# Kernel optimization log

Hardware: AMD Instinct MI355X
Metric: run time of the kernel (lower is better)

Reference implementation:

```python
import jax, jax.numpy as jnp
import numpy as np

N_NODES = 100000


def setup_inputs() -> dict:
    key = jax.random.key(0)
    k1, k2, k3, k4, k5 = jax.random.split(key, 5)
    n_edges = 3200000
    in_f, out_f = 256, 256
    X = jax.random.normal(k1, (N_NODES, in_f), dtype=jnp.float32)
    edge_src = jax.random.randint(k2, (n_edges,), 0, N_NODES, dtype=jnp.int32)
    edge_dst = jax.random.randint(k3, (n_edges,), 0, N_NODES, dtype=jnp.int32)
    edge_val = jax.random.uniform(k4, (n_edges,), dtype=jnp.float32)
    # kaiming-uniform-like init for weight (out_f, in_f)
    bound = np.sqrt(6.0 / in_f)
    W = jax.random.uniform(k5, (out_f, in_f), dtype=jnp.float32, minval=-bound, maxval=bound)
    b = jnp.zeros((out_f,), dtype=jnp.float32)
    return {"X": X, "edge_src": edge_src, "edge_dst": edge_dst,
            "edge_val": edge_val, "W": W, "b": b}


def reference(X, edge_src, edge_dst, edge_val, W, b):
    # S = A @ X, where A is COO sparse: A[src, dst] = val
    # gather neighbor features, scale by edge value, scatter-add to src rows
    msgs = edge_val[:, None] * X[edge_dst]              # [E, in_f]
    S = jax.ops.segment_sum(msgs, edge_src, num_segments=N_NODES)  # [N, in_f]
    # dense projection + bias: (A X) W^T + b
    return S @ W.T + b
```

## Files before the change

### kernel.cpp

```cpp
#include <hip/hip_runtime.h>

#define NNODES 100000
#define F 256
#define NBKT ((NNODES + 127) / 128)
#define BKT_CAP 5120
#define CHUNK_A 8192

typedef unsigned short u16;
typedef unsigned int   u32;
typedef __attribute__((ext_vector_type(8))) short short8v;
typedef __attribute__((ext_vector_type(8))) unsigned short ushort8;
typedef __attribute__((ext_vector_type(4))) float f32x4;
typedef __attribute__((ext_vector_type(2))) float f32x2;

__device__ __forceinline__ u16 f2bf(float f) {
    u32 u = __float_as_uint(f);
    u32 r = u + 0x7FFFu + ((u >> 16) & 1u);
    return (u16)(r >> 16);
}

__global__ __launch_bounds__(256) void cast_w_init(const float* __restrict__ W,
                                                   u16* __restrict__ Wb,
                                                   int* __restrict__ cur) {
    int i = blockIdx.x * 256 + threadIdx.x;
    if (i < F * F / 4) {
        float4 w = ((const float4*)W)[i];
        ushort4 o;
        o.x = f2bf(w.x); o.y = f2bf(w.y); o.z = f2bf(w.z); o.w = f2bf(w.w);
        ((ushort4*)Wb)[i] = o;
    }
    if (i < NBKT) cur[i] = i * BKT_CAP;
}

__global__ __launch_bounds__(256) void cast_x(const float* __restrict__ X,
                                              u16* __restrict__ Xb, int total4) {
    int i = blockIdx.x * 256 + threadIdx.x;
    if (i >= total4) return;
    float4 x = ((const float4*)X)[i];
    ushort4 o;
    o.x = f2bf(x.x); o.y = f2bf(x.y); o.z = f2bf(x.z); o.w = f2bf(x.w);
    ((ushort4*)Xb)[i] = o;
}

__global__ __launch_bounds__(256) void gemm_mfma(const u16* __restrict__ Xb,
                                                 const u16* __restrict__ Wb,
                                                 u16* __restrict__ Yb) {
    __shared__ u16 As[128 * 128];
    __shared__ u16 Bs[128 * 128];
    const int wv   = threadIdx.x >> 6;
    const int lane = threadIdx.x & 63;
    const int lm   = lane & 15;
    const int kg   = lane >> 4;
    const int m0   = blockIdx.x * 128;
    const int n0   = blockIdx.y * 128;

    f32x4 acc[2][8];
#pragma unroll
    for (int t = 0; t < 2; ++t)
#pragma unroll
        for (int u = 0; u < 8; ++u) acc[t][u] = (f32x4){0.f, 0.f, 0.f, 0.f};

#pragma unroll
    for (int kt = 0; kt < 2; ++kt) {
        if (kt) __syncthreads();
#pragma unroll
        for (int i = 0; i < 8; ++i) {
            int q   = i * 256 + threadIdx.x;
            int row = q >> 4;
            int cs  = (q & 15) ^ (row & 7);
            size_t goff = (size_t)row * 512 + kt * 256 + cs * 16;
            *(ushort8*)&As[q * 8] = *(const ushort8*)((const char*)Xb + (size_t)m0 * 512 + goff);
            *(ushort8*)&Bs[q * 8] = *(const ushort8*)((const char*)Wb + (size_t)n0 * 512 + goff);
        }
        __syncthreads();
#pragma unroll
        for (int s = 0; s < 4; ++s) {
            short8v aF[2];
#pragma unroll
            for (int t = 0; t < 2; ++t) {
                int r = wv * 32 + t * 16 + lm;
                int c = (s * 4 + kg) ^ (r & 7);
                aF[t] = *(const short8v*)&As[r * 128 + c * 8];
            }
            short8v bF[8];
#pragma unroll
            for (int u = 0; u < 8; ++u) {
                int r = u * 16 + lm;
                int c = (s * 4 + kg) ^ (r & 7);
                bF[u] = *(const short8v*)&Bs[r * 128 + c * 8];
            }
#pragma unroll
            for (int t = 0; t < 2; ++t)
#pragma unroll
                for (int u = 0; u < 8; ++u)
                    acc[t][u] = __builtin_amdgcn_mfma_f32_16x16x32_bf16(aF[t], bF[u], acc[t][u], 0, 0, 0);
        }
    }

#pragma unroll
    for (int t = 0; t < 2; ++t) {
        int rbase = m0 + wv * 32 + t * 16 + kg * 4;
#pragma unroll
        for (int i = 0; i < 4; ++i) {
            int row = rbase + i;
            if (row < NNODES) {
#pragma unroll
                for (int u = 0; u < 8; ++u)
                    Yb[(size_t)row * F + n0 + u * 16 + lm] = f2bf(acc[t][u][i]);
            }
        }
    }
}

__global__ __launch_bounds__(256) void bin_edges(const int* __restrict__ src,
                                                 const int* __restrict__ dst,
                                                 const float* __restrict__ val,
                                                 int* __restrict__ cur,
                                                 int2* __restrict__ temp,
                                                 int n_edges) {
    __shared__ int hist[NBKT];
    __shared__ int bas[NBKT];
    const int e0 = blockIdx.x * CHUNK_A;
    for (int i = threadIdx.x; i < NBKT; i += 256) hist[i] = 0;
    __syncthreads();

    u32 lpk[32];
#pragma unroll
    for (int k = 0; k < 32; ++k) {
        int e = e0 + k * 256 + threadIdx.x;
        if (e < n_edges) {
            int s = src[e];
            int bkt = s >> 7;
            int l = atomicAdd(&hist[bkt], 1);
            lpk[k] = (u32)l | ((u32)(s & 127) << 13) | ((u32)bkt << 20);
        }
    }
    __syncthreads();
    for (int i = threadIdx.x; i < NBKT; i += 256) {
        int c = hist[i];
        bas[i] = c ? atomicAdd(&cur[i], c) : 0;
    }
    __syncthreads();
#pragma unroll
    for (int k = 0; k < 32; ++k) {
        int e = e0 + k * 256 + threadIdx.x;
        if (e < n_edges) {
            u32 p   = lpk[k];
            int bkt = (int)(p >> 20);
            int pos = bas[bkt] + (int)(p & 0x1FFFu);
            int sl  = (int)((p >> 13) & 127u);
            temp[pos] = make_int2((sl << 20) | dst[e], __float_as_int(val[e]));
        }
    }
}

__global__ __launch_bounds__(256) void sort_bucket(const int* __restrict__ cur,
                                                   const int2* __restrict__ temp,
                                                   int2* __restrict__ pack,
                                                   int2* __restrict__ nodeseg) {
    __shared__ int2 tl[BKT_CAP];
    __shared__ int h[128];
    __shared__ int curl[128];
    const int b = blockIdx.x;
    const int base = b * BKT_CAP;
    int cnt = cur[b] - base;
    if (cnt > BKT_CAP) cnt = BKT_CAP;
    const int tid = threadIdx.x;

    if (tid < 128) h[tid] = 0;
    __syncthreads();
    for (int j = tid; j < cnt; j += 256) {
        int2 t = temp[base + j];
        tl[j] = t;
        atomicAdd(&h[t.x >> 20], 1);
    }
    __syncthreads();
    for (int off = 1; off < 128; off <<= 1) {
        int x = 0;
        if (tid < 128 && tid >= off) x = h[tid - off];
        __syncthreads();
        if (tid < 128) h[tid] += x;
        __syncthreads();
    }
    if (tid < 128) {
        int incl = h[tid];
        int prev = tid ? h[tid - 1] : 0;
        curl[tid] = base + prev;
        int node = b * 128 + tid;
        if (node < NNODES) nodeseg[node] = make_int2(base + prev, base + incl);
    }
    __syncthreads();
    for (int j = tid; j < cnt; j += 256) {
        int2 p = tl[j];
        int loc = p.x >> 20;
        int pos = atomicAdd(&curl[loc], 1);
        pack[pos] = make_int2((p.x & 0xFFFFF) << 9, p.y);
    }
}

__global__ __launch_bounds__(256) void gather_nodes(const int2* __restrict__ nodeseg,
                                                    const int2* __restrict__ pack,
                                                    const u16* __restrict__ Yb,
                                                    const float* __restrict__ bias,
                                                    float* __restrict__ out) {
    int node = blockIdx.x * 4 + (threadIdx.x >> 6);
    if (node >= NNODES) return;
    const int lane = threadIdx.x & 63;
    const int half = lane >> 5;
    const int l5   = lane & 31;
    const u32 loff = (u32)l5 * 16u;
    const char* Ybc = (const char*)Yb;

    int2 seg = nodeseg[node];
    const int beg = seg.x, end = seg.y;

    f32x2 acc2[4];
#pragma unroll
    for (int i = 0; i < 4; ++i) acc2[i] = (f32x2){0.f, 0.f};

    for (int j = beg; j < end; j += 16) {
        u32 off[8];
        float v[8];
        ushort8 y[8];
#pragma unroll
        for (int q = 0; q < 8; ++q) {
            int idx = j + 2 * q + half;
            int safe = idx < end ? idx : end - 1;
            long long raw = __builtin_nontemporal_load((const long long*)&pack[safe]);
            off[q] = (u32)((unsigned long long)raw & 0xFFFFFFFFull);
            v[q] = (idx < end) ? __int_as_float((int)(raw >> 32)) : 0.f;
        }
#pragma unroll
        for (int q = 0; q < 8; ++q)
            y[q] = *(const ushort8*)(Ybc + (off[q] + loff));
#pragma unroll
        for (int q = 0; q < 8; ++q) {
            f32x2 vv; vv[0] = v[q]; vv[1] = v[q];
            const u32* yp = (const u32*)&y[q];
#pragma unroll
            for (int i = 0; i < 4; ++i) {
                u32 pb = yp[i];
                f32x2 yy;
                yy[0] = __uint_as_float(pb << 16);
                yy[1] = __uint_as_float(pb & 0xFFFF0000u);
                acc2[i] = __builtin_elementwise_fma(yy, vv, acc2[i]);
            }
        }
    }

    float acc[8];
#pragma unroll
    for (int i = 0; i < 4; ++i) { acc[2 * i] = acc2[i][0]; acc[2 * i + 1] = acc2[i][1]; }
#pragma unroll
    for (int i = 0; i < 8; ++i) acc[i] += __shfl_xor(acc[i], 32);

    const int col = l5 * 8 + half * 4;
    float4 bv = *(const float4*)&bias[col];
    f32x4 o;
    o[0] = acc[half * 4 + 0] + bv.x;
    o[1] = acc[half * 4 + 1] + bv.y;
    o[2] = acc[half * 4 + 2] + bv.z;
    o[3] = acc[half * 4 + 3] + bv.w;
    __builtin_nontemporal_store(o, (f32x4*)&out[(size_t)node * F + col]);
}

extern "C" void kernel_launch(void* const* d_in, const int* in_sizes, int n_in,
                              void* d_out, int out_size, void* d_ws, size_t ws_size,
                              hipStream_t stream) {
    const float* X        = (const float*)d_in[0];
    const int*   edge_src = (const int*)d_in[1];
    const int*   edge_dst = (const int*)d_in[2];
    const float* edge_val = (const float*)d_in[3];
    const float* W        = (const float*)d_in[4];
    const float* b        = (const float*)d_in[5];
    float*       out      = (float*)d_out;
    const int n_edges     = in_sizes[1];

    char* base = (char*)d_ws;
    const size_t ybBytes   = (size_t)NNODES * F * sizeof(u16);
    const size_t packBytes = (size_t)NBKT * BKT_CAP * sizeof(int2);
    u16*  Yb      = (u16*)base;
    int2* pack    = (int2*)(base + ybBytes);
    int2* temp    = (int2*)(base + ybBytes + packBytes);
    u16*  Xb      = (u16*)pack;
    u16*  Wb      = (u16*)(base + ybBytes + 2 * packBytes);
    int2* nodeseg = (int2*)((char*)Wb + (size_t)F * F * sizeof(u16));
    int*  cur     = (int*)(nodeseg + NNODES);

    cast_w_init<<<(F * F / 4 + 255) / 256, 256, 0, stream>>>(W, Wb, cur);
    int xt4 = NNODES * F / 4;
    cast_x<<<(xt4 + 255) / 256, 256, 0, stream>>>(X, Xb, xt4);

    dim3 ggrid((NNODES + 127) / 128, F / 128);
    gemm_mfma<<<ggrid, 256, 0, stream>>>(Xb, Wb, Yb);

    bin_edges<<<(n_edges + CHUNK_A - 1) / CHUNK_A, 256, 0, stream>>>(edge_src, edge_dst, edge_val,
                                                                     cur, temp, n_edges);
    sort_bucket<<<NBKT, 256, 0, stream>>>(cur, temp, pack, nodeseg);

    gather_nodes<<<(NNODES + 3) / 4, 256, 0, stream>>>(nodeseg, pack, Yb, b, out);
}
```

Baseline: 552.6 us.

## Replace atomic bucket binning with count, scan, write passes

Global atomicAdd reservation of bucket offsets is replaced by three passes: a per-block histogram that writes counts to global memory, a per-bucket exclusive scan across blocks, and a write pass that reads the precomputed offsets. Offsets become deterministic and global atomic contention on the cursor array goes away. In exchange there are two extra kernel launches, src is read a second time, and the count matrix makes an extra trip through global memory. Bucket capacity drops slightly, and writes past capacity are now dropped explicitly.

```diff
diff --git a/kernel.cpp b/kernel.cpp
--- a/kernel.cpp
+++ b/kernel.cpp
@@ -3,7 +3,7 @@
 #define NNODES 100000
 #define F 256
 #define NBKT ((NNODES + 127) / 128)
-#define BKT_CAP 5120
+#define BKT_CAP 5000
 #define CHUNK_A 8192
 
 typedef unsigned short u16;
@@ -19,17 +19,14 @@
     return (u16)(r >> 16);
 }
 
-__global__ __launch_bounds__(256) void cast_w_init(const float* __restrict__ W,
-                                                   u16* __restrict__ Wb,
-                                                   int* __restrict__ cur) {
+__global__ __launch_bounds__(256) void cast_w(const float* __restrict__ W,
+                                              u16* __restrict__ Wb) {
     int i = blockIdx.x * 256 + threadIdx.x;
-    if (i < F * F / 4) {
-        float4 w = ((const float4*)W)[i];
-        ushort4 o;
-        o.x = f2bf(w.x); o.y = f2bf(w.y); o.z = f2bf(w.z); o.w = f2bf(w.w);
-        ((ushort4*)Wb)[i] = o;
-    }
-    if (i < NBKT) cur[i] = i * BKT_CAP;
+    if (i >= F * F / 4) return;
+    float4 w = ((const float4*)W)[i];
+    ushort4 o;
+    o.x = f2bf(w.x); o.y = f2bf(w.y); o.z = f2bf(w.z); o.w = f2bf(w.w);
+    ((ushort4*)Wb)[i] = o;
 }
 
 __global__ __launch_bounds__(256) void cast_x(const float* __restrict__ X,
@@ -112,18 +109,55 @@
     }
 }
 
-__global__ __launch_bounds__(256) void bin_edges(const int* __restrict__ src,
+
+__global__ __launch_bounds__(256) void bin_count(const int* __restrict__ src,
+                                                 int* __restrict__ counts,
+                                                 int n_edges) {
+    __shared__ int hist[NBKT];
+    const int e0 = blockIdx.x * CHUNK_A;
+    for (int i = threadIdx.x; i < NBKT; i += 256) hist[i] = 0;
+    __syncthreads();
+#pragma unroll
+    for (int k = 0; k < 32; ++k) {
+        int e = e0 + k * 256 + threadIdx.x;
+        if (e < n_edges) atomicAdd(&hist[src[e] >> 7], 1);
+    }
+    __syncthreads();
+    for (int i = threadIdx.x; i < NBKT; i += 256)
+        counts[(size_t)blockIdx.x * NBKT + i] = hist[i];
+}
+
+__global__ __launch_bounds__(256) void bin_scan(int* __restrict__ counts,
+                                                int* __restrict__ bktcnt, int nblk) {
+    __shared__ int s[512];
+    const int b = blockIdx.x;
+    const int t = threadIdx.x;
+    int v0 = (t < nblk)       ? counts[(size_t)t * NBKT + b]         : 0;
+    int v1 = (t + 256 < nblk) ? counts[(size_t)(t + 256) * NBKT + b] : 0;
+    s[t] = v0; s[t + 256] = v1;
+    __syncthreads();
+    for (int off = 1; off < 512; off <<= 1) {
+        int a0 = (t >= off) ? s[t - off] : 0;
+        int a1 = (t + 256 >= off) ? s[t + 256 - off] : 0;
+        __syncthreads();
+        s[t] += a0; s[t + 256] += a1;
+        __syncthreads();
+    }
+    const int base = b * BKT_CAP;
+    if (t < nblk)       counts[(size_t)t * NBKT + b]         = base + s[t] - v0;
+    if (t + 256 < nblk) counts[(size_t)(t + 256) * NBKT + b] = base + s[t + 256] - v1;
+    if (t == 255) bktcnt[b] = s[511];
+}
+
+__global__ __launch_bounds__(256) void bin_write(const int* __restrict__ src,
                                                  const int* __restrict__ dst,
                                                  const float* __restrict__ val,
-                                                 int* __restrict__ cur,
-                                                 int2* __restrict__ temp,
-                                                 int n_edges) {
+                                                 const int* __restrict__ counts,
+                                                 int2* __restrict__ temp, int n_edges) {
     __shared__ int hist[NBKT];
-    __shared__ int bas[NBKT];
     const int e0 = blockIdx.x * CHUNK_A;
     for (int i = threadIdx.x; i < NBKT; i += 256) hist[i] = 0;
     __syncthreads();
-
     u32 lpk[32];
 #pragma unroll
     for (int k = 0; k < 32; ++k) {
@@ -135,26 +169,21 @@
             lpk[k] = (u32)l | ((u32)(s & 127) << 13) | ((u32)bkt << 20);
         }
     }
-    __syncthreads();
-    for (int i = threadIdx.x; i < NBKT; i += 256) {
-        int c = hist[i];
-        bas[i] = c ? atomicAdd(&cur[i], c) : 0;
-    }
-    __syncthreads();
 #pragma unroll
     for (int k = 0; k < 32; ++k) {
         int e = e0 + k * 256 + threadIdx.x;
         if (e < n_edges) {
             u32 p   = lpk[k];
             int bkt = (int)(p >> 20);
-            int pos = bas[bkt] + (int)(p & 0x1FFFu);
+            int pos = counts[(size_t)blockIdx.x * NBKT + bkt] + (int)(p & 0x1FFFu);
             int sl  = (int)((p >> 13) & 127u);
-            temp[pos] = make_int2((sl << 20) | dst[e], __float_as_int(val[e]));
-        }
-    }
-}
-
-__global__ __launch_bounds__(256) void sort_bucket(const int* __restrict__ cur,
+            if (pos < (bkt + 1) * BKT_CAP)
+                temp[pos] = make_int2((sl << 20) | dst[e], __float_as_int(val[e]));
+        }
+    }
+}
+
+__global__ __launch_bounds__(256) void sort_bucket(const int* __restrict__ bktcnt,
                                                    const int2* __restrict__ temp,
                                                    int2* __restrict__ pack,
                                                    int2* __restrict__ nodeseg) {
@@ -163,7 +192,7 @@
     __shared__ int curl[128];
     const int b = blockIdx.x;
     const int base = b * BKT_CAP;
-    int cnt = cur[b] - base;
+    int cnt = bktcnt[b];
     if (cnt > BKT_CAP) cnt = BKT_CAP;
     const int tid = threadIdx.x;
 
@@ -275,6 +304,7 @@
     const float* b        = (const float*)d_in[5];
     float*       out      = (float*)d_out;
     const int n_edges     = in_sizes[1];
+    const int nblk        = (n_edges + CHUNK_A - 1) / CHUNK_A;
 
     char* base = (char*)d_ws;
     const size_t ybBytes   = (size_t)NNODES * F * sizeof(u16);
@@ -285,18 +315,20 @@
     u16*  Xb      = (u16*)pack;
     u16*  Wb      = (u16*)(base + ybBytes + 2 * packBytes);
     int2* nodeseg = (int2*)((char*)Wb + (size_t)F * F * sizeof(u16));
-    int*  cur     = (int*)(nodeseg + NNODES);
-
-    cast_w_init<<<(F * F / 4 + 255) / 256, 256, 0, stream>>>(W, Wb, cur);
+    int*  counts  = (int*)(nodeseg + NNODES);
+    int*  bktcnt  = counts + (size_t)nblk * NBKT;
+
+    cast_w<<<(F * F / 4 + 255) / 256, 256, 0, stream>>>(W, Wb);
     int xt4 = NNODES * F / 4;
     cast_x<<<(xt4 + 255) / 256, 256, 0, stream>>>(X, Xb, xt4);
 
     dim3 ggrid((NNODES + 127) / 128, F / 128);
     gemm_mfma<<<ggrid, 256, 0, stream>>>(Xb, Wb, Yb);
 
-    bin_edges<<<(n_edges + CHUNK_A - 1) / CHUNK_A, 256, 0, stream>>>(edge_src, edge_dst, edge_val,
-                                                                     cur, temp, n_edges);
-    sort_bucket<<<NBKT, 256, 0, stream>>>(cur, temp, pack, nodeseg);
+    bin_count<<<nblk, 256, 0, stream>>>(edge_src, counts, n_edges);
+    bin_scan<<<NBKT, 256, 0, stream>>>(counts, bktcnt, nblk);
+    bin_write<<<nblk, 256, 0, stream>>>(edge_src, edge_dst, edge_val, counts, temp, n_edges);
+    sort_bucket<<<NBKT, 256, 0, stream>>>(bktcnt, temp, pack, nodeseg);
 
     gather_nodes<<<(NNODES + 3) / 4, 256, 0, stream>>>(nodeseg, pack, Yb, b, out);
 }
```

After: 570.1 us. 1.03x slower.
